# Optimization experiments

Hardware: AMD Instinct MI355X
Metric: run time of the kernel (lower is better)

## Reference

```python
import jax, jax.numpy as jnp
import numpy as np

N = 8192
TOKEN_DIM = 384
K = 16
D_IN = 2 * (TOKEN_DIM + 3)  # 774


def setup_inputs() -> dict:
    key = jax.random.key(0)
    k1, k2, k3, k4, k5, k6 = jax.random.split(key, 6)
    xyz = jax.random.normal(k1, (N, 3), dtype=jnp.float32)
    feat = jax.random.normal(k2, (N, TOKEN_DIM), dtype=jnp.float32)
    W1 = jax.random.normal(k3, (D_IN, TOKEN_DIM), dtype=jnp.float32) / np.sqrt(D_IN)
    b1 = jax.random.normal(k4, (TOKEN_DIM,), dtype=jnp.float32) * 0.01
    W2 = jax.random.normal(k5, (TOKEN_DIM, 3), dtype=jnp.float32) / np.sqrt(TOKEN_DIM)
    b2 = jax.random.normal(k6, (3,), dtype=jnp.float32) * 0.01
    return {"xyz": xyz, "feat": feat, "W1": W1, "b1": b1, "W2": W2, "b2": b2}


def _knn_idx(xyz, k):
    # pairwise squared distances [N, N]; loop=False -> exclude self via +inf diag
    sq = jnp.sum(xyz * xyz, axis=-1)
    d2 = sq[:, None] + sq[None, :] - 2.0 * (xyz @ xyz.T)
    n = xyz.shape[0]
    d2 = jnp.where(jnp.eye(n, dtype=bool), jnp.inf, d2)
    _, idx = jax.lax.top_k(-d2, k)  # idx[i] = k nearest neighbors (sources) of target i
    return idx


def reference(xyz, feat, W1, b1, W2, b2):
    idx = _knn_idx(xyz, K)                      # [N, K] int32
    x = jnp.concatenate([feat, xyz], axis=-1)   # [N, D] with D = token_dim + 3
    x_j = x[idx]                                # [N, K, D] gathered neighbor feats
    x_i = x[:, None, :]                         # [N, 1, D]
    # EdgeConv message: nn(cat([x_i, x_j - x_i]))
    e = jnp.concatenate([jnp.broadcast_to(x_i, x_j.shape), x_j - x_i], axis=-1)  # [N, K, 2D]
    h = jax.nn.relu(jnp.einsum('nkd,df->nkf', e, W1) + b1)   # [N, K, token_dim]
    m = jnp.einsum('nkf,fo->nko', h, W2) + b2                # [N, K, 3]
    agg = jnp.max(m, axis=1)                                 # max aggregation over neighbors
    return xyz + agg
```

## Files before the change

kernel.cpp:

```cpp
#include <hip/hip_runtime.h>
#include <hip/hip_bf16.h>


#define N 8192
#define TD 384
#define KNN 16
#define DX 387
#define KP 416
#define NF 768
#define INFF __builtin_inff()

typedef __attribute__((ext_vector_type(8))) short short8;
typedef __attribute__((ext_vector_type(4))) float f32x4;
typedef __attribute__((ext_vector_type(2))) float f32x2;


__device__ __forceinline__ f32x2 pk_mul(f32x2 a, f32x2 b) {
    f32x2 r; asm("v_pk_mul_f32 %0, %1, %2" : "=v"(r) : "v"(a), "v"(b)); return r;
}
__device__ __forceinline__ f32x2 pk_add(f32x2 a, f32x2 b) {
    f32x2 r; asm("v_pk_add_f32 %0, %1, %2" : "=v"(r) : "v"(a), "v"(b)); return r;
}
__device__ __forceinline__ f32x2 pk_sub(f32x2 a, f32x2 b) {
    f32x2 r; asm("v_pk_add_f32 %0, %1, %2 neg_lo:[0,1] neg_hi:[0,1]" : "=v"(r) : "v"(a), "v"(b)); return r;
}
__device__ __forceinline__ f32x2 pk_fma(f32x2 a, f32x2 b, f32x2 c) {
    f32x2 r; asm("v_pk_fma_f32 %0, %1, %2, %3" : "=v"(r) : "v"(a), "v"(b), "v"(c)); return r;
}

__device__ __forceinline__ void dist4(f32x2 qx, f32x2 qy, f32x2 qz, f32x2 qw,
                                      f32x2 x01, f32x2 x23, f32x2 y01, f32x2 y23,
                                      f32x2 z01, f32x2 z23, f32x2 s01, f32x2 s23,
                                      f32x2& d01, f32x2& d23) {
    f32x2 dot01 = pk_fma(qz, z01, pk_fma(qy, y01, pk_mul(qx, x01)));
    f32x2 dot23 = pk_fma(qz, z23, pk_fma(qy, y23, pk_mul(qx, x23)));
    d01 = pk_sub(pk_add(qw, s01), pk_add(dot01, dot01));
    d23 = pk_sub(pk_add(qw, s23), pk_add(dot23, dot23));
}

__device__ __forceinline__ int xbin(float x) {
    int b = (int)((x + 4.0f) * 32.0f);
    return b < 0 ? 0 : (b > 255 ? 255 : b);
}


__global__ void __launch_bounds__(128) prep_all(const float* __restrict__ feat,
                                                const float* __restrict__ xyz,
                                                const float* __restrict__ W1,
                                                __hip_bfloat16* __restrict__ Xb,
                                                __hip_bfloat16* __restrict__ Wpt,
                                                int* __restrict__ cut) {
    int b = blockIdx.x;
    int t = threadIdx.x;
    if (b < N) {
        if (t < 96) {
            float4 f = reinterpret_cast<const float4*>(feat + (size_t)b*TD)[t];
            __hip_bfloat16 h[4] = {__float2bfloat16(f.x), __float2bfloat16(f.y),
                                   __float2bfloat16(f.z), __float2bfloat16(f.w)};
            *reinterpret_cast<ulonglong1*>(Xb + b*KP + t*4) = *reinterpret_cast<ulonglong1*>(h);
        } else if (t == 96) {
            for (int d = TD; d < KP; ++d) {
                float v = (d < DX) ? xyz[b*3 + (d - TD)] : 0.f;
                Xb[b*KP + d] = __float2bfloat16(v);
            }
        }
    } else if (b < N + NF) {
        int f = b - N;
        for (int k = t; k < KP; k += 128) {
            float v = 0.f;
            if (k < DX) {
                if (f < TD) v = W1[k*TD + f] - W1[(DX+k)*TD + f];
                else        v = W1[(DX+k)*TD + (f - TD)];
            }
            Wpt[f*KP + k] = __float2bfloat16(v);
        }
    } else {
        cut[t] = 0;
        cut[t + 128] = 0;
    }
}


__global__ void __launch_bounds__(256) assign_kernel(const float* __restrict__ xyz,
                                                     int* __restrict__ cut,
                                                     int* __restrict__ tlo,
                                                     int* __restrict__ thi,
                                                     float* __restrict__ stile) {
    __shared__ int hcnt[256];
    __shared__ int base[256];
    __shared__ int stlo[32], sthi[32];
    const int t = threadIdx.x;

    hcnt[t] = 0;
    if (t < 32) { stlo[t] = 255; sthi[t] = 0; }
    __syncthreads();

    #pragma unroll
    for (int c = 0; c < 32; ++c) {
        atomicAdd(&hcnt[xbin(xyz[(t + c*256)*3])], 1);
    }
    __syncthreads();

    const int v = hcnt[t];
    base[t] = v;
    __syncthreads();
    for (int off = 1; off < 256; off <<= 1) {
        int add = (t >= off) ? base[t - off] : 0;
        __syncthreads();
        base[t] += add;
        __syncthreads();
    }
    const int end = base[t], start = end - v;
    __syncthreads();
    base[t] = start;
    __syncthreads();

    if (blockIdx.x == 0) {
        if (v > 0) {
            for (int x = start >> 8; x <= (end - 1) >> 8; ++x) {
                atomicMin(&stlo[x], t);
                atomicMax(&sthi[x], t);
            }
        }
        __syncthreads();
        if (t < 32) { tlo[t] = stlo[t]; thi[t] = sthi[t]; }
    }

    const int i = blockIdx.x * 256 + t;
    float x = xyz[i*3+0], y = xyz[i*3+1], z = xyz[i*3+2];
    int bin = xbin(x);
    int pos = base[bin] + atomicAdd(&cut[bin], 1);
    float sq = __fadd_rn(__fadd_rn(__fmul_rn(x,x), __fmul_rn(y,y)), __fmul_rn(z,z));
    float* tp = stile + (pos >> 8) * 1280 + (pos & 255);
    tp[0] = x; tp[256] = y; tp[512] = z; tp[768] = sq;
    reinterpret_cast<int*>(tp)[1024] = i;
}


__device__ __forceinline__ float dpp_shr1_f(float v) {
    return __uint_as_float((unsigned)__builtin_amdgcn_update_dpp(
        (int)__float_as_uint(v), (int)__float_as_uint(v), 0x111, 0xF, 0xF, false));
}
__device__ __forceinline__ int dpp_shr1_i(int v) {
    return __builtin_amdgcn_update_dpp(v, v, 0x111, 0xF, 0xF, false);
}
__device__ __forceinline__ float rdlane_f(float v, int src) {
    return __uint_as_float(__builtin_amdgcn_readlane(__float_as_uint(v), src));
}

__device__ __forceinline__ void insert16p(float dv, int cjv, float Tq,
                                          float& ld, int& li, float& Tl, int lane) {
    unsigned long long m = __ballot((dv <= Tq) && (dv < Tl));
    while (m) {
        int src = (int)__ffsll(m) - 1;
        float cd = rdlane_f(dv, src);
        int   cj = __builtin_amdgcn_readlane(cjv, src);
        bool lt = (ld < cd) || (ld == cd && li < cj);
        int pos = (int)__popcll(__ballot(lt) & 0xFFFFull);
        float ud = dpp_shr1_f(ld);
        int   ui = dpp_shr1_i(li);
        ld = (lane == pos) ? cd : ((lane > pos) ? ud : ld);
        li = (lane == pos) ? cj : ((lane > pos) ? ui : li);
        Tl = rdlane_f(ld, 15);
        m &= ~(1ull << src);
        m &= __ballot(dv < Tl);
    }
}


__global__ void __launch_bounds__(256, 8) knn_kernel(const float* __restrict__ stile,
                                                     const int* __restrict__ tlo,
                                                     const int* __restrict__ thi,
                                                     int* __restrict__ knn) {
    const int lane = threadIdx.x & 63;
    const int wv   = threadIdx.x >> 6;
    const int s    = blockIdx.x * 4 + wv;
    const int tq   = s >> 8;
    const int sl   = (s & 255) >> 2;
    const int slot = s & 3;

    const float* qp = stile + tq*1280 + (s & 255);
    const float qx = qp[0], qy = qp[256], qz = qp[512], qw = qp[768];
    const int   qi = reinterpret_cast<const int*>(qp)[1024];
    const f32x2 qx2 = {qx,qx}, qy2 = {qy,qy}, qz2 = {qz,qz}, qw2 = {qw,qw};

    const float* lbase = stile + lane*4;
    const bool is_self_lane = (lane == sl);

    float mn = INFF;
    int lo = tq - 2; if (lo < 0) lo = 0; if (lo > 27) lo = 27;
    #pragma unroll
    for (int tt = 0; tt < 5; ++tt) {
        const int t = lo + tt;
        const float* tp = lbase + t*1280;
        float4 X = *(const float4*)(tp);
        float4 Y = *(const float4*)(tp + 256);
        float4 Z = *(const float4*)(tp + 512);
        float4 S = *(const float4*)(tp + 768);
        f32x2 x01 = {X.x,X.y}, x23 = {X.z,X.w};
        f32x2 y01 = {Y.x,Y.y}, y23 = {Y.z,Y.w};
        f32x2 z01 = {Z.x,Z.y}, z23 = {Z.z,Z.w};
        f32x2 s01 = {S.x,S.y}, s23 = {S.z,S.w};
        f32x2 d01, d23;
        dist4(qx2, qy2, qz2, qw2, x01, x23, y01, y23, z01, z23, s01, s23, d01, d23);
        if ((t == tq) && is_self_lane) {
            if      (slot == 0) d01[0] = INFF;
            else if (slot == 1) d01[1] = INFF;
            else if (slot == 2) d23[0] = INFF;
            else                d23[1] = INFF;
        }
        mn = fminf(mn, fminf(fminf(d01[0], d01[1]), fminf(d23[0], d23[1])));
    }

    float T;
    {
        unsigned x = __float_as_uint(mn);
        unsigned ub = ((int)x < 0) ? ~x : (x | 0x80000000u);
        unsigned long long alive = ~0ull;
        int need = KNN;
        for (int b = 31; b >= 0; --b) {
            unsigned long long ones  = __ballot(((ub >> b) & 1u) != 0u);
            unsigned long long zeros = alive & ~ones;
            int cz = (int)__popcll(zeros);
            bool tz = (cz >= need);
            alive = tz ? zeros : (alive & ones);
            need  = tz ? need : (need - cz);
        }
        T = fmaxf(rdlane_f(mn, (int)__ffsll(alive) - 1), 0.f);
    }

    unsigned mask;
    {
        const int ti = lane & 31;
        const int bl = tlo[ti], bh = thi[ti];
        const float xlo = (bl == 0)   ? -1e30f : (bl * 0.03125f - 4.0f);
        const float xhi = (bh == 255) ?  1e30f : ((bh + 1) * 0.03125f - 4.0f);
        float gap = fmaxf(0.f, fmaxf(xlo - qx, qx - xhi));
        bool gate = (gap * gap <= T + 1e-3f);
        mask = (unsigned)__ballot(gate && (lane < 32));
    }

    float ld = INFF;
    int   li = -1;
    float Tl = INFF;

    while (mask) {
        const int t = (int)__ffs(mask) - 1;
        mask &= mask - 1;
        const float* tp = lbase + t*1280;
        float4 X = *(const float4*)(tp);
        float4 Y = *(const float4*)(tp + 256);
        float4 Z = *(const float4*)(tp + 512);
        float4 S = *(const float4*)(tp + 768);
        int4   I = *(const int4*)(tp + 1024);
        f32x2 x01 = {X.x,X.y}, x23 = {X.z,X.w};
        f32x2 y01 = {Y.x,Y.y}, y23 = {Y.z,Y.w};
        f32x2 z01 = {Z.x,Z.y}, z23 = {Z.z,Z.w};
        f32x2 s01 = {S.x,S.y}, s23 = {S.z,S.w};
        f32x2 d01, d23;
        dist4(qx2, qy2, qz2, qw2, x01, x23, y01, y23, z01, z23, s01, s23, d01, d23);
        if ((t == tq) && is_self_lane) {
            if      (slot == 0) d01[0] = INFF;
            else if (slot == 1) d01[1] = INFF;
            else if (slot == 2) d23[0] = INFF;
            else                d23[1] = INFF;
        }
        float tmin = fminf(fminf(d01[0], d01[1]), fminf(d23[0], d23[1]));
        if (__ballot(tmin <= T)) {
            insert16p(d01[0], I.x, T, ld, li, Tl, lane);
            insert16p(d01[1], I.y, T, ld, li, Tl, lane);
            insert16p(d23[0], I.z, T, ld, li, Tl, lane);
            insert16p(d23[1], I.w, T, ld, li, Tl, lane);
        }
    }

    if (lane < KNN) knn[qi*KNN + lane] = li;
}


__global__ void __launch_bounds__(64) gemm_kernel(const __hip_bfloat16* __restrict__ Xb,
                                                  const __hip_bfloat16* __restrict__ Wpt,
                                                  const float* __restrict__ b1,
                                                  __hip_bfloat16* __restrict__ Ub,
                                                  __hip_bfloat16* __restrict__ Vb) {
    const int lane = threadIdx.x;
    const int i0   = blockIdx.x * 64;
    const int f0   = blockIdx.y * 64;
    const int lm   = lane & 15;
    const int lk   = (lane >> 4) * 8;

    f32x4 acc[4][4];
    #pragma unroll
    for (int r = 0; r < 4; ++r)
        #pragma unroll
        for (int c = 0; c < 4; ++c)
            acc[r][c] = (f32x4){0.f, 0.f, 0.f, 0.f};

    const __hip_bfloat16* xbase = Xb  + (size_t)(i0 + lm) * KP + lk;
    const __hip_bfloat16* wbase = Wpt + (size_t)(f0 + lm) * KP + lk;

    #pragma unroll
    for (int kk = 0; kk < 13; ++kk) {
        short8 a[4], b[4];
        #pragma unroll
        for (int r = 0; r < 4; ++r)
            a[r] = *reinterpret_cast<const short8*>(xbase + (size_t)r*16*KP + kk*32);
        #pragma unroll
        for (int c = 0; c < 4; ++c)
            b[c] = *reinterpret_cast<const short8*>(wbase + (size_t)c*16*KP + kk*32);
        #pragma unroll
        for (int r = 0; r < 4; ++r)
            #pragma unroll
            for (int c = 0; c < 4; ++c)
                acc[r][c] = __builtin_amdgcn_mfma_f32_16x16x32_bf16(a[r], b[c], acc[r][c], 0, 0, 0);
    }

    const bool isU = (f0 < TD);
    __hip_bfloat16* outb = isU ? (Ub + f0) : (Vb + (f0 - TD));
    float bias[4] = {0.f, 0.f, 0.f, 0.f};
    if (isU) {
        #pragma unroll
        for (int c = 0; c < 4; ++c) bias[c] = b1[f0 + c*16 + lm];
    }
    const int crow = (lane >> 4) * 4;
    #pragma unroll
    for (int r = 0; r < 4; ++r)
        #pragma unroll
        for (int c = 0; c < 4; ++c)
            #pragma unroll
            for (int q = 0; q < 4; ++q)
                outb[(size_t)(i0 + r*16 + crow + q) * TD + c*16 + lm] =
                    __float2bfloat16(acc[r][c][q] + bias[c]);
}


__device__ __forceinline__ float bflo(unsigned w) { return __uint_as_float(w << 16); }
__device__ __forceinline__ float bfhi(unsigned w) { return __uint_as_float(w & 0xFFFF0000u); }

template<int CTRL>
__device__ __forceinline__ float dppf(float v) {
    return __uint_as_float((unsigned)__builtin_amdgcn_update_dpp(
        0, (int)__float_as_uint(v), CTRL, 0xF, 0xF, true));
}

__global__ void __launch_bounds__(256) final_kernel(const __hip_bfloat16* __restrict__ Ub,
                                                    const __hip_bfloat16* __restrict__ Vb,
                                                    const int* __restrict__ knn,
                                                    const float* __restrict__ xyz,
                                                    const float* __restrict__ W2,
                                                    const float* __restrict__ b2,
                                                    float* __restrict__ out) {
    const int lane = threadIdx.x & 63;
    const int wv   = threadIdx.x >> 6;
    const int i    = blockIdx.x * 4 + wv;
    const int d0   = lane * 6;

    int jreg = knn[i*KNN + (lane & 15)];

    float u[6], w2l[6][3];
    {
        const unsigned* rowU = reinterpret_cast<const unsigned*>(Ub + (size_t)i * TD) + lane*3;
        unsigned a0 = rowU[0], a1 = rowU[1], a2 = rowU[2];
        u[0] = bflo(a0); u[1] = bfhi(a0);
        u[2] = bflo(a1); u[3] = bfhi(a1);
        u[4] = bflo(a2); u[5] = bfhi(a2);
    }
    #pragma unroll
    for (int t = 0; t < 6; ++t)
        #pragma unroll
        for (int c = 0; c < 3; ++c) w2l[t][c] = W2[(d0 + t)*3 + c];

    const unsigned* vbase = reinterpret_cast<const unsigned*>(Vb);
    const int voff = lane * 3;

    float pk0[16], pk1[16], pk2[16];
    unsigned va[2][4][3];

    #pragma unroll
    for (int t = 0; t < 4; ++t) {
        int j = __builtin_amdgcn_readlane(jreg, t);
        const unsigned* rv = vbase + (size_t)j * 192 + voff;
        va[0][t][0] = rv[0]; va[0][t][1] = rv[1]; va[0][t][2] = rv[2];
    }
    __builtin_amdgcn_sched_barrier(0);

    #pragma unroll
    for (int b = 0; b < 4; ++b) {
        if (b < 3) {
            #pragma unroll
            for (int t = 0; t < 4; ++t) {
                int j = __builtin_amdgcn_readlane(jreg, (b+1)*4 + t);
                const unsigned* rv = vbase + (size_t)j * 192 + voff;
                va[(b+1)&1][t][0] = rv[0];
                va[(b+1)&1][t][1] = rv[1];
                va[(b+1)&1][t][2] = rv[2];
            }
            __builtin_amdgcn_sched_barrier(0);
        }
        #pragma unroll
        for (int t = 0; t < 4; ++t) {
            const int kk = b*4 + t;
            unsigned a0 = va[b&1][t][0], a1 = va[b&1][t][1], a2 = va[b&1][t][2];
            float v0 = bflo(a0), v1 = bfhi(a0);
            float v2 = bflo(a1), v3 = bfhi(a1);
            float v4 = bflo(a2), v5 = bfhi(a2);
            float h0 = fmaxf(u[0] + v0, 0.f), h1 = fmaxf(u[1] + v1, 0.f);
            float h2 = fmaxf(u[2] + v2, 0.f), h3 = fmaxf(u[3] + v3, 0.f);
            float h4 = fmaxf(u[4] + v4, 0.f), h5 = fmaxf(u[5] + v5, 0.f);
            float s0 = 0.f, s1 = 0.f, s2 = 0.f;
            s0 = fmaf(h0, w2l[0][0], s0); s1 = fmaf(h0, w2l[0][1], s1); s2 = fmaf(h0, w2l[0][2], s2);
            s0 = fmaf(h1, w2l[1][0], s0); s1 = fmaf(h1, w2l[1][1], s1); s2 = fmaf(h1, w2l[1][2], s2);
            s0 = fmaf(h2, w2l[2][0], s0); s1 = fmaf(h2, w2l[2][1], s1); s2 = fmaf(h2, w2l[2][2], s2);
            s0 = fmaf(h3, w2l[3][0], s0); s1 = fmaf(h3, w2l[3][1], s1); s2 = fmaf(h3, w2l[3][2], s2);
            s0 = fmaf(h4, w2l[4][0], s0); s1 = fmaf(h4, w2l[4][1], s1); s2 = fmaf(h4, w2l[4][2], s2);
            s0 = fmaf(h5, w2l[5][0], s0); s1 = fmaf(h5, w2l[5][1], s1); s2 = fmaf(h5, w2l[5][2], s2);
            pk0[kk] = s0; pk1[kk] = s1; pk2[kk] = s2;
        }
    }

    #pragma unroll
    for (int kk = 0; kk < 16; ++kk) {
        float r0 = pk0[kk], r1 = pk1[kk], r2 = pk2[kk];
        r0 += dppf<0x121>(r0); r1 += dppf<0x121>(r1); r2 += dppf<0x121>(r2);
        r0 += dppf<0x122>(r0); r1 += dppf<0x122>(r1); r2 += dppf<0x122>(r2);
        r0 += dppf<0x124>(r0); r1 += dppf<0x124>(r1); r2 += dppf<0x124>(r2);
        r0 += dppf<0x128>(r0); r1 += dppf<0x128>(r1); r2 += dppf<0x128>(r2);
        r0 += __shfl_xor(r0, 16); r1 += __shfl_xor(r1, 16); r2 += __shfl_xor(r2, 16);
        r0 += __shfl_xor(r0, 32); r1 += __shfl_xor(r1, 32); r2 += __shfl_xor(r2, 32);
        pk0[kk] = r0; pk1[kk] = r1; pk2[kk] = r2;
    }
    float mx0 = pk0[0], mx1 = pk1[0], mx2 = pk2[0];
    #pragma unroll
    for (int kk = 1; kk < 16; ++kk) {
        mx0 = fmaxf(mx0, pk0[kk]);
        mx1 = fmaxf(mx1, pk1[kk]);
        mx2 = fmaxf(mx2, pk2[kk]);
    }

    if (lane == 0) {
        out[i*3+0] = xyz[i*3+0] + mx0 + b2[0];
        out[i*3+1] = xyz[i*3+1] + mx1 + b2[1];
        out[i*3+2] = xyz[i*3+2] + mx2 + b2[2];
    }
}


extern "C" void kernel_launch(void* const* d_in, const int* in_sizes, int n_in,
                              void* d_out, int out_size, void* d_ws, size_t ws_size,
                              hipStream_t stream) {
    const float* xyz  = (const float*)d_in[0];
    const float* feat = (const float*)d_in[1];
    const float* W1   = (const float*)d_in[2];
    const float* b1   = (const float*)d_in[3];
    const float* W2   = (const float*)d_in[4];
    const float* b2   = (const float*)d_in[5];
    float* out = (float*)d_out;

    char* ws = (char*)d_ws;
    int*            knn   = (int*)(ws + 0);
    float*          stile = (float*)(ws + 524288);
    __hip_bfloat16* Xb    = (__hip_bfloat16*)(ws + 688128);
    __hip_bfloat16* Wpt   = (__hip_bfloat16*)(ws + 7503872);
    __hip_bfloat16* Ub    = (__hip_bfloat16*)(ws + 8142848);
    __hip_bfloat16* Vb    = (__hip_bfloat16*)(ws + 14434304);
    int*            cut   = (int*)(ws + 20725760);
    int*            thi   = (int*)(ws + 20726784);
    int*            tlo   = (int*)(ws + 20726912);

    prep_all     <<<dim3(N + NF + 1),  dim3(128), 0, stream>>>(feat, xyz, W1, Xb, Wpt, cut);
    assign_kernel<<<dim3(N/256),       dim3(256), 0, stream>>>(xyz, cut, tlo, thi, stile);
    knn_kernel   <<<dim3(N/4),         dim3(256), 0, stream>>>(stile, tlo, thi, knn);
    gemm_kernel  <<<dim3(N/64, NF/64), dim3(64),  0, stream>>>(Xb, Wpt, b1, Ub, Vb);
    final_kernel <<<dim3(N/4),         dim3(256), 0, stream>>>(Ub, Vb, knn, xyz, W2, b2, out);
}
```

Baseline: 87.37 us.

## Replace serial top-16 insertion with LDS candidate buffer and radix select

The per-candidate serial insertion into a wave-wide sorted list is replaced. Candidates under the threshold are compacted into a per-wave LDS buffer of up to 128 entries, and the 16 smallest are then chosen with a ballot-based radix select over distance, with a second radix pass on index to break ties. This removes the long serialized readlane/DPP insertion loop, at the cost of extra LDS traffic and a fixed 32-step select. Output neighbors are no longer written in sorted order. Candidates beyond 128 are silently dropped, which risks wrong results if the threshold lets too many through.

New measurement: 85.96 us. No clear change (-1.6%).

```diff
diff --git a/kernel.cpp b/kernel.cpp
--- a/kernel.cpp
+++ b/kernel.cpp
@@ -137,34 +137,12 @@
 }
 
 
-__device__ __forceinline__ float dpp_shr1_f(float v) {
-    return __uint_as_float((unsigned)__builtin_amdgcn_update_dpp(
-        (int)__float_as_uint(v), (int)__float_as_uint(v), 0x111, 0xF, 0xF, false));
-}
-__device__ __forceinline__ int dpp_shr1_i(int v) {
-    return __builtin_amdgcn_update_dpp(v, v, 0x111, 0xF, 0xF, false);
-}
 __device__ __forceinline__ float rdlane_f(float v, int src) {
     return __uint_as_float(__builtin_amdgcn_readlane(__float_as_uint(v), src));
 }
-
-__device__ __forceinline__ void insert16p(float dv, int cjv, float Tq,
-                                          float& ld, int& li, float& Tl, int lane) {
-    unsigned long long m = __ballot((dv <= Tq) && (dv < Tl));
-    while (m) {
-        int src = (int)__ffsll(m) - 1;
-        float cd = rdlane_f(dv, src);
-        int   cj = __builtin_amdgcn_readlane(cjv, src);
-        bool lt = (ld < cd) || (ld == cd && li < cj);
-        int pos = (int)__popcll(__ballot(lt) & 0xFFFFull);
-        float ud = dpp_shr1_f(ld);
-        int   ui = dpp_shr1_i(li);
-        ld = (lane == pos) ? cd : ((lane > pos) ? ud : ld);
-        li = (lane == pos) ? cj : ((lane > pos) ? ui : li);
-        Tl = rdlane_f(ld, 15);
-        m &= ~(1ull << src);
-        m &= __ballot(dv < Tl);
-    }
+__device__ __forceinline__ unsigned udmap(float x) {
+    unsigned u = __float_as_uint(x);
+    return ((int)u < 0) ? ~u : (u | 0x80000000u);
 }
 
 
@@ -172,6 +150,7 @@
                                                      const int* __restrict__ tlo,
                                                      const int* __restrict__ thi,
                                                      int* __restrict__ knn) {
+    __shared__ unsigned sbuf[4][128][2];
     const int lane = threadIdx.x & 63;
     const int wv   = threadIdx.x >> 6;
     const int s    = blockIdx.x * 4 + wv;
@@ -214,10 +193,10 @@
 
     float T;
     {
-        unsigned x = __float_as_uint(mn);
-        unsigned ub = ((int)x < 0) ? ~x : (x | 0x80000000u);
+        unsigned ub = udmap(mn);
         unsigned long long alive = ~0ull;
         int need = KNN;
+        #pragma unroll
         for (int b = 31; b >= 0; --b) {
             unsigned long long ones  = __ballot(((ub >> b) & 1u) != 0u);
             unsigned long long zeros = alive & ~ones;
@@ -240,9 +219,21 @@
         mask = (unsigned)__ballot(gate && (lane < 32));
     }
 
-    float ld = INFF;
-    int   li = -1;
-    float Tl = INFF;
+    int cnt = 0;
+    const unsigned long long ltm = (1ull << lane) - 1;
+
+    auto push = [&](float dv, int idx) {
+        bool pred = (dv <= T);
+        unsigned long long bal = __ballot(pred);
+        if (bal) {
+            int posn = cnt + (int)__popcll(bal & ltm);
+            if (pred && posn < 128) {
+                sbuf[wv][posn][0] = udmap(dv);
+                sbuf[wv][posn][1] = (unsigned)idx;
+            }
+            cnt += (int)__popcll(bal);
+        }
+    };
 
     while (mask) {
         const int t = (int)__ffs(mask) - 1;
@@ -267,14 +258,67 @@
         }
         float tmin = fminf(fminf(d01[0], d01[1]), fminf(d23[0], d23[1]));
         if (__ballot(tmin <= T)) {
-            insert16p(d01[0], I.x, T, ld, li, Tl, lane);
-            insert16p(d01[1], I.y, T, ld, li, Tl, lane);
-            insert16p(d23[0], I.z, T, ld, li, Tl, lane);
-            insert16p(d23[1], I.w, T, ld, li, Tl, lane);
-        }
-    }
-
-    if (lane < KNN) knn[qi*KNN + lane] = li;
+            push(d01[0], I.x);
+            push(d01[1], I.y);
+            push(d23[0], I.z);
+            push(d23[1], I.w);
+        }
+    }
+
+    asm volatile("s_waitcnt lgkmcnt(0)" ::: "memory");
+    const int M = (cnt > 128) ? 128 : cnt;
+    unsigned ud1 = 0xFFFFFFFFu, id1 = 0xFFFFFFFFu;
+    unsigned ud2 = 0xFFFFFFFFu, id2 = 0xFFFFFFFFu;
+    if (lane < M)      { ud1 = sbuf[wv][lane][0];      id1 = sbuf[wv][lane][1]; }
+    if (lane + 64 < M) { ud2 = sbuf[wv][lane + 64][0]; id2 = sbuf[wv][lane + 64][1]; }
+
+    unsigned long long alive1 = __ballot(lane < M);
+    unsigned long long alive2 = __ballot(lane + 64 < M);
+    int need = KNN;
+    #pragma unroll
+    for (int b = 31; b >= 0; --b) {
+        unsigned long long on1 = __ballot(((ud1 >> b) & 1u) != 0u);
+        unsigned long long on2 = __ballot(((ud2 >> b) & 1u) != 0u);
+        unsigned long long z1 = alive1 & ~on1;
+        unsigned long long z2 = alive2 & ~on2;
+        int cz = (int)__popcll(z1) + (int)__popcll(z2);
+        bool tz = (cz >= need);
+        alive1 = tz ? z1 : (alive1 & on1);
+        alive2 = tz ? z2 : (alive2 & on2);
+        need   = tz ? need : (need - cz);
+    }
+    unsigned v16;
+    if (alive1) v16 = (unsigned)__builtin_amdgcn_readlane((int)ud1, (int)__ffsll(alive1) - 1);
+    else        v16 = (unsigned)__builtin_amdgcn_readlane((int)ud2, (int)__ffsll(alive2) - 1);
+
+    const int nt = (int)__popcll(alive1) + (int)__popcll(alive2);
+    const bool all_ties = (nt <= need);
+    unsigned vidx = 0xFFFFFFFFu;
+    if (!all_ties) {
+        unsigned long long a1 = alive1, a2 = alive2;
+        int nd = need;
+        for (int b = 31; b >= 0; --b) {
+            unsigned long long on1 = __ballot(((id1 >> b) & 1u) != 0u);
+            unsigned long long on2 = __ballot(((id2 >> b) & 1u) != 0u);
+            unsigned long long z1 = a1 & ~on1;
+            unsigned long long z2 = a2 & ~on2;
+            int cz = (int)__popcll(z1) + (int)__popcll(z2);
+            bool tz = (cz >= nd);
+            a1 = tz ? z1 : (a1 & on1);
+            a2 = tz ? z2 : (a2 & on2);
+            nd = tz ? nd : (nd - cz);
+        }
+        if (a1) vidx = (unsigned)__builtin_amdgcn_readlane((int)id1, (int)__ffsll(a1) - 1);
+        else    vidx = (unsigned)__builtin_amdgcn_readlane((int)id2, (int)__ffsll(a2) - 1);
+    }
+
+    bool sel1 = (lane < M)      && ((ud1 < v16) || ((ud1 == v16) && (all_ties || (id1 <= vidx))));
+    bool sel2 = (lane + 64 < M) && ((ud2 < v16) || ((ud2 == v16) && (all_ties || (id2 <= vidx))));
+    unsigned long long bs1 = __ballot(sel1);
+    if (sel1) knn[qi*KNN + (int)__popcll(bs1 & ltm)] = (int)id1;
+    const int c1 = (int)__popcll(bs1);
+    unsigned long long bs2 = __ballot(sel2);
+    if (sel2) knn[qi*KNN + c1 + (int)__popcll(bs2 & ltm)] = (int)id2;
 }
 
 
```
